# Performance work log

Hardware: AMD Instinct MI355X
Metric: run time of the kernel (lower is better)

The kernel has to match this reference:

```python
import jax, jax.numpy as jnp
import numpy as np

NUM_CLASSES = 1000
EMBED_DIM = 1024
BATCH = 32768
FACTOR = 0.3


def setup_inputs() -> dict:
    key = jax.random.key(0)
    k1, k2, k3 = jax.random.split(key, 3)
    embed = jax.random.normal(k1, (BATCH, EMBED_DIM), dtype=jnp.float32)
    y = jax.random.randint(k2, (BATCH,), 0, NUM_CLASSES, dtype=jnp.int64)
    centroid = jax.random.normal(k3, (NUM_CLASSES, EMBED_DIM), dtype=jnp.float32)
    return {"embed": embed, "y": y, "centroid": centroid}


def reference(embed, y, centroid):
    # Per-class sum of embeddings: equivalent to eye(C)[y].T @ embed,
    # done as a scatter-add (segment_sum) instead of a dense one-hot matmul.
    sums = jax.ops.segment_sum(embed, y, num_segments=NUM_CLASSES)  # [C, D]
    counts = jax.ops.segment_sum(
        jnp.ones((embed.shape[0],), dtype=embed.dtype), y, num_segments=NUM_CLASSES
    )  # [C] == weight.sum(dim=1)
    cur_centroid = sums / counts[:, None]  # per-class mean
    new_centroid = FACTOR * cur_centroid + (1.0 - FACTOR) * centroid
    return new_centroid
```

## Files before the change

kernel.cpp:

```cpp
#include <hip/hip_runtime.h>


#define BATCH       32768
#define EMBED_DIM   1024
#define NUM_CLASSES 1000
#define FACTOR      0.3f


__global__ __launch_bounds__(1024) void zero_kernel(int* __restrict__ cnt)
{
    cnt[threadIdx.x] = 0;
}

__global__ __launch_bounds__(256) void hist_kernel(const int* __restrict__ y,
                                                   int* __restrict__ cnt)
{
    const int i = blockIdx.x * 256 + threadIdx.x;
    atomicAdd(&cnt[y[i]], 1);
}

__global__ __launch_bounds__(1024) void scan_kernel(int* __restrict__ cnt,
                                                    int* __restrict__ offs)
{
    __shared__ int s[1024];
    const int t = threadIdx.x;
    const int v = (t < NUM_CLASSES) ? cnt[t] : 0;
    s[t] = v;
    __syncthreads();
    #pragma unroll
    for (int d = 1; d < 1024; d <<= 1) {
        const int x = (t >= d) ? s[t - d] : 0;
        __syncthreads();
        s[t] += x;
        __syncthreads();
    }
    const int excl = s[t] - v;
    if (t < NUM_CLASSES) { offs[t] = excl; cnt[t] = excl; }
    if (t == 1023) offs[NUM_CLASSES] = s[1023];
}

__global__ __launch_bounds__(256) void scatter_kernel(const int* __restrict__ y,
                                                      int* __restrict__ cursor,
                                                      int* __restrict__ rowlist)
{
    const int i = blockIdx.x * 256 + threadIdx.x;
    const int c = y[i];
    const int pos = atomicAdd(&cursor[c], 1);
    rowlist[pos] = i;
}

__global__ __launch_bounds__(256) void gather_kernel(
    const float* __restrict__ embed,
    const float* __restrict__ centroid,
    const int*   __restrict__ offs,
    const int*   __restrict__ rowlist,
    float*       __restrict__ out)
{
    const int c   = blockIdx.x;
    const int tid = threadIdx.x;
    const int d0  = tid * 4;

    const int start = offs[c];
    const int m     = offs[c + 1] - start;

    __shared__ int rows[256];

    float4 acc = make_float4(0.f, 0.f, 0.f, 0.f);

    for (int base = 0; base < m; base += 256) {
        const int k = min(256, m - base);
        if (tid < k) rows[tid] = rowlist[start + base + tid];
        __syncthreads();

        int j = 0;
        for (; j + 4 <= k; j += 4) {
            const int r0 = rows[j + 0];
            const int r1 = rows[j + 1];
            const int r2 = rows[j + 2];
            const int r3 = rows[j + 3];
            const float4 v0 = *reinterpret_cast<const float4*>(embed + (size_t)r0 * EMBED_DIM + d0);
            const float4 v1 = *reinterpret_cast<const float4*>(embed + (size_t)r1 * EMBED_DIM + d0);
            const float4 v2 = *reinterpret_cast<const float4*>(embed + (size_t)r2 * EMBED_DIM + d0);
            const float4 v3 = *reinterpret_cast<const float4*>(embed + (size_t)r3 * EMBED_DIM + d0);
            acc.x += v0.x; acc.y += v0.y; acc.z += v0.z; acc.w += v0.w;
            acc.x += v1.x; acc.y += v1.y; acc.z += v1.z; acc.w += v1.w;
            acc.x += v2.x; acc.y += v2.y; acc.z += v2.z; acc.w += v2.w;
            acc.x += v3.x; acc.y += v3.y; acc.z += v3.z; acc.w += v3.w;
        }
        for (; j < k; ++j) {
            const int r = rows[j];
            const float4 v = *reinterpret_cast<const float4*>(embed + (size_t)r * EMBED_DIM + d0);
            acc.x += v.x; acc.y += v.y; acc.z += v.z; acc.w += v.w;
        }
        __syncthreads();
    }

    const float inv = 1.0f / (float)m;
    const size_t o = (size_t)c * EMBED_DIM + d0;
    const float4 cen = *reinterpret_cast<const float4*>(centroid + o);
    float4 res;
    res.x = FACTOR * (acc.x * inv) + (1.0f - FACTOR) * cen.x;
    res.y = FACTOR * (acc.y * inv) + (1.0f - FACTOR) * cen.y;
    res.z = FACTOR * (acc.z * inv) + (1.0f - FACTOR) * cen.z;
    res.w = FACTOR * (acc.w * inv) + (1.0f - FACTOR) * cen.w;
    *reinterpret_cast<float4*>(out + o) = res;
}

extern "C" void kernel_launch(void* const* d_in, const int* in_sizes, int n_in,
                              void* d_out, int out_size, void* d_ws, size_t ws_size,
                              hipStream_t stream) {
    const float* embed    = (const float*)d_in[0];
    const int*   y        = (const int*)d_in[1];
    const float* centroid = (const float*)d_in[2];
    float*       out      = (float*)d_out;

    int* ws      = (int*)d_ws;
    int* cnt     = ws;
    int* offs    = ws + 1024;
    int* rowlist = ws + 2048;

    zero_kernel   <<<1, 1024, 0, stream>>>(cnt);
    hist_kernel   <<<BATCH / 256, 256, 0, stream>>>(y, cnt);
    scan_kernel   <<<1, 1024, 0, stream>>>(cnt, offs);
    scatter_kernel<<<BATCH / 256, 256, 0, stream>>>(y, cnt, rowlist);
    gather_kernel <<<NUM_CLASSES, 256, 0, stream>>>(embed, centroid, offs, rowlist, out);
}
```

Baseline: 220.9 us.

## Fuse histogram, scan and scatter into one single-block prep kernel

Replaces the zero, histogram, scan and scatter kernels with one 1024-thread block that builds the histogram and scatter cursors with shared-memory atomics. This removes three kernel launches and the global atomics. It also unrolls the gather loop to issue 8 row loads at a time instead of 4, for more memory-level parallelism. The cost is that y is processed serially by a single workgroup, and the order within rowlist stays nondeterministic.

```diff
diff --git a/kernel.cpp b/kernel.cpp
--- a/kernel.cpp
+++ b/kernel.cpp
@@ -7,46 +7,54 @@
 #define FACTOR      0.3f
 
 
-__global__ __launch_bounds__(1024) void zero_kernel(int* __restrict__ cnt)
+__global__ __launch_bounds__(1024) void prep_kernel(const int* __restrict__ y,
+                                                    int* __restrict__ offs,
+                                                    int* __restrict__ rowlist)
 {
-    cnt[threadIdx.x] = 0;
-}
+    __shared__ int hist[1024];
+    __shared__ int scan[1024];
+    const int t = threadIdx.x;
 
-__global__ __launch_bounds__(256) void hist_kernel(const int* __restrict__ y,
-                                                   int* __restrict__ cnt)
-{
-    const int i = blockIdx.x * 256 + threadIdx.x;
-    atomicAdd(&cnt[y[i]], 1);
-}
+    hist[t] = 0;
+    __syncthreads();
 
-__global__ __launch_bounds__(1024) void scan_kernel(int* __restrict__ cnt,
-                                                    int* __restrict__ offs)
-{
-    __shared__ int s[1024];
-    const int t = threadIdx.x;
-    const int v = (t < NUM_CLASSES) ? cnt[t] : 0;
-    s[t] = v;
+    #pragma unroll
+    for (int kk = 0; kk < 8; ++kk) {
+        const int idx = kk * 4096 + t * 4;
+        const int4 v = *reinterpret_cast<const int4*>(y + idx);
+        atomicAdd(&hist[v.x], 1);
+        atomicAdd(&hist[v.y], 1);
+        atomicAdd(&hist[v.z], 1);
+        atomicAdd(&hist[v.w], 1);
+    }
+    __syncthreads();
+
+    const int cnt = hist[t];
+    scan[t] = cnt;
     __syncthreads();
     #pragma unroll
     for (int d = 1; d < 1024; d <<= 1) {
-        const int x = (t >= d) ? s[t - d] : 0;
+        const int x = (t >= d) ? scan[t - d] : 0;
         __syncthreads();
-        s[t] += x;
+        scan[t] += x;
         __syncthreads();
     }
-    const int excl = s[t] - v;
-    if (t < NUM_CLASSES) { offs[t] = excl; cnt[t] = excl; }
-    if (t == 1023) offs[NUM_CLASSES] = s[1023];
-}
+    const int excl = scan[t] - cnt;
+    hist[t] = excl;
+    if (t < NUM_CLASSES) offs[t] = excl;
+    if (t == 0) offs[NUM_CLASSES] = BATCH;
+    __syncthreads();
 
-__global__ __launch_bounds__(256) void scatter_kernel(const int* __restrict__ y,
-                                                      int* __restrict__ cursor,
-                                                      int* __restrict__ rowlist)
-{
-    const int i = blockIdx.x * 256 + threadIdx.x;
-    const int c = y[i];
-    const int pos = atomicAdd(&cursor[c], 1);
-    rowlist[pos] = i;
+    #pragma unroll
+    for (int kk = 0; kk < 8; ++kk) {
+        const int idx = kk * 4096 + t * 4;
+        const int4 v = *reinterpret_cast<const int4*>(y + idx);
+        int p;
+        p = atomicAdd(&hist[v.x], 1); rowlist[p] = idx + 0;
+        p = atomicAdd(&hist[v.y], 1); rowlist[p] = idx + 1;
+        p = atomicAdd(&hist[v.z], 1); rowlist[p] = idx + 2;
+        p = atomicAdd(&hist[v.w], 1); rowlist[p] = idx + 3;
+    }
 }
 
 __global__ __launch_bounds__(256) void gather_kernel(
@@ -73,23 +81,24 @@
         __syncthreads();
 
         int j = 0;
-        for (; j + 4 <= k; j += 4) {
-            const int r0 = rows[j + 0];
-            const int r1 = rows[j + 1];
-            const int r2 = rows[j + 2];
-            const int r3 = rows[j + 3];
-            const float4 v0 = *reinterpret_cast<const float4*>(embed + (size_t)r0 * EMBED_DIM + d0);
-            const float4 v1 = *reinterpret_cast<const float4*>(embed + (size_t)r1 * EMBED_DIM + d0);
-            const float4 v2 = *reinterpret_cast<const float4*>(embed + (size_t)r2 * EMBED_DIM + d0);
-            const float4 v3 = *reinterpret_cast<const float4*>(embed + (size_t)r3 * EMBED_DIM + d0);
-            acc.x += v0.x; acc.y += v0.y; acc.z += v0.z; acc.w += v0.w;
-            acc.x += v1.x; acc.y += v1.y; acc.z += v1.z; acc.w += v1.w;
-            acc.x += v2.x; acc.y += v2.y; acc.z += v2.z; acc.w += v2.w;
-            acc.x += v3.x; acc.y += v3.y; acc.z += v3.z; acc.w += v3.w;
+        for (; j + 8 <= k; j += 8) {
+            float4 v[8];
+            #pragma unroll
+            for (int u = 0; u < 8; ++u) {
+                const int r = rows[j + u];
+                v[u] = *reinterpret_cast<const float4*>(
+                    embed + (size_t)r * EMBED_DIM + d0);
+            }
+            #pragma unroll
+            for (int u = 0; u < 8; ++u) {
+                acc.x += v[u].x; acc.y += v[u].y;
+                acc.z += v[u].z; acc.w += v[u].w;
+            }
         }
         for (; j < k; ++j) {
             const int r = rows[j];
-            const float4 v = *reinterpret_cast<const float4*>(embed + (size_t)r * EMBED_DIM + d0);
+            const float4 v = *reinterpret_cast<const float4*>(
+                embed + (size_t)r * EMBED_DIM + d0);
             acc.x += v.x; acc.y += v.y; acc.z += v.z; acc.w += v.w;
         }
         __syncthreads();
@@ -115,13 +124,9 @@
     float*       out      = (float*)d_out;
 
     int* ws      = (int*)d_ws;
-    int* cnt     = ws;
-    int* offs    = ws + 1024;
-    int* rowlist = ws + 2048;
+    int* offs    = ws;
+    int* rowlist = ws + 1024;
 
-    zero_kernel   <<<1, 1024, 0, stream>>>(cnt);
-    hist_kernel   <<<BATCH / 256, 256, 0, stream>>>(y, cnt);
-    scan_kernel   <<<1, 1024, 0, stream>>>(cnt, offs);
-    scatter_kernel<<<BATCH / 256, 256, 0, stream>>>(y, cnt, rowlist);
-    gather_kernel <<<NUM_CLASSES, 256, 0, stream>>>(embed, centroid, offs, rowlist, out);
+    prep_kernel  <<<1, 1024, 0, stream>>>(y, offs, rowlist);
+    gather_kernel<<<NUM_CLASSES, 256, 0, stream>>>(embed, centroid, offs, rowlist, out);
 }
```

Measured after the change: 224.8 us. Within noise of the previous version (+1.8%).
